# Kernel optimization log

Measured on AMD Instinct MI355X. Metric: run time of the kernel, lower is better.

The kernel has to match this reference:

```python
import jax, jax.numpy as jnp
import numpy as np

N, E = 50000, 800000
IN, EF, D, H = 128, 128, 32, 8
CUTOFF = 5.0
NEG_SLOPE = 0.2


def setup_inputs() -> dict:
    key = jax.random.key(0)
    ks = jax.random.split(key, 14)
    s = 0.1  # param init scale (xavier-ish)
    return {
        "nfeat": jax.random.normal(ks[0], (N, IN), jnp.float32),
        "efeat": jax.random.normal(ks[1], (E, EF), jnp.float32),
        "rij": jax.random.uniform(ks[2], (E,), jnp.float32) * 6.0,
        "src": jax.random.randint(ks[3], (E,), 0, N, jnp.int32),
        "dst": jax.random.randint(ks[4], (E,), 0, N, jnp.int32),
        "W_fc": jax.random.normal(ks[5], (H * D, IN), jnp.float32) * s,
        "W_e1": jax.random.normal(ks[6], (D, EF), jnp.float32) * s,
        "b_e1": jnp.zeros((D,), jnp.float32),
        "W_e2": jax.random.normal(ks[7], (H * D, D), jnp.float32) * s,
        "b_e2": jnp.zeros((H * D,), jnp.float32),
        "attn_l": jax.random.normal(ks[8], (1, H, D), jnp.float32) * s,
        "attn_r": jax.random.normal(ks[9], (1, H, D), jnp.float32) * s,
        "attn_edge": jax.random.normal(ks[10], (1, H, D), jnp.float32) * s,
        "bias": jnp.zeros((H * D,), jnp.float32),
    }


def _ssp(x):
    # ShiftedSoftplus: softplus(x) - log(2)
    return jax.nn.softplus(x) - jnp.log(2.0).astype(x.dtype)


def _cosine_cutoff(r):
    return jnp.where(r < CUTOFF, 0.5 * (jnp.cos(jnp.pi * r / CUTOFF) + 1.0), 0.0)


def reference(nfeat, efeat, rij, src, dst, W_fc, W_e1, b_e1, W_e2, b_e2,
              attn_l, attn_r, attn_edge, bias):
    n = nfeat.shape[0]
    feat = (nfeat @ W_fc.T).reshape(n, H, D)                # [N,H,D]
    ef = _ssp(efeat @ W_e1.T + b_e1)                         # [E,D]
    ef = _ssp(ef @ W_e2.T + b_e2)                            # [E,H*D]
    ef = (_cosine_cutoff(rij)[:, None] * ef).reshape(-1, H, D)  # [E,H,D]

    el = jnp.sum(feat * attn_l, axis=-1)                     # [N,H]
    er = jnp.sum(feat * attn_r, axis=-1)                     # [N,H]
    ee = jnp.sum(ef * attn_edge, axis=-1)                    # [E,H]

    e = jax.nn.leaky_relu(el[src] + er[dst] + ee, NEG_SLOPE)  # [E,H]
    # edge softmax over destination-node neighborhoods
    emax = jax.ops.segment_max(e, dst, num_segments=n)
    ex = jnp.exp(e - emax[dst])
    esum = jax.ops.segment_sum(ex, dst, num_segments=n)
    a = ex / esum[dst]                                       # [E,H]
    a = a * ee                                               # a * dis

    m = feat[src] * a[:, :, None]                            # [E,H,D]
    rst = jax.ops.segment_sum(m, dst, num_segments=n)        # [N,H,D]
    rst = rst + bias.reshape(1, H, D)
    return rst
```

## Files before the change

### kernel.cpp

```cpp
#include <hip/hip_runtime.h>
#include <hip/hip_bf16.h>

#define NN 50000
#define NE 800000
#define HD 256
#define KIN 128
#define SCAN_B 49

#define FB_FEAT 1563
#define FB_FILL 1024
#define FB_EDGE 12500

typedef __attribute__((ext_vector_type(8))) short bf16x8;
typedef __attribute__((ext_vector_type(8))) short short8v;
typedef __attribute__((ext_vector_type(4))) float f32x4;

static __device__ __forceinline__ short f2b(float f){
  union { __hip_bfloat16 h; short s; } u;
  u.h = __float2bfloat16(f);
  return u.s;
}
static __device__ __forceinline__ float b2f(short s){
  union { __hip_bfloat16 h; short s; } u;
  u.s = s;
  return __bfloat162float(u.h);
}
static __device__ __forceinline__ unsigned packbf(float a, float b){
  union { short s[2]; unsigned u; } z;
  z.s[0] = f2b(a); z.s[1] = f2b(b);
  return z.u;
}
static __device__ __forceinline__ float sspf(float x){
#if __has_builtin(__builtin_amdgcn_exp2f) && __has_builtin(__builtin_amdgcn_logf)
  const float t = __builtin_amdgcn_exp2f(fabsf(x) * -1.4426950408889634f);
  return fmaf(__builtin_amdgcn_logf(1.0f + t) - 1.0f, 0.69314718055994531f, fmaxf(x, 0.0f));
#else
  const float t = __expf(-fabsf(x));
  return fmaxf(x, 0.0f) + __logf(1.0f + t) - 0.69314718055994531f;
#endif
}

__global__ void k_cvh(const float* __restrict__ wfc, const float* __restrict__ we1,
                      const float* __restrict__ we2,
                      const float* __restrict__ be2, const float* __restrict__ attn_e,
                      const int* __restrict__ dst,
                      short* __restrict__ wfcb, short* __restrict__ we1b,
                      short* __restrict__ we2b, float* __restrict__ w2pk,
                      int* __restrict__ deg){
  const int i = blockIdx.x*256 + threadIdx.x;
  if (i < HD*KIN) wfcb[i] = f2b(wfc[i]);
  if (i < 32*KIN) we1b[i] = f2b(we1[i]);
  if (i < HD*32)  we2b[i] = f2b(we2[i]);
  if (i < 512){
    const int cht = i >> 5, r = i & 31, lq = r >> 3, j = r & 7;
    const int ch = cht*16 + lq*4 + (j & 3);
    w2pk[i] = (j < 4) ? be2[ch] : attn_e[ch];
  }
  for (int e = i; e < NE; e += gridDim.x*blockDim.x)
    atomicAdd(&deg[dst[e]], 1);
}

__global__ __launch_bounds__(1024) void k_scanA(const int* __restrict__ deg,
                                                int* __restrict__ bsum){
  __shared__ int ws[16];
  const int t = threadIdx.x;
  const int i = blockIdx.x*1024 + t;
  int v = (i < NN) ? deg[i] : 0;
#pragma unroll
  for (int m=1;m<64;m<<=1) v += __shfl_xor(v, m, 64);
  if ((t & 63) == 0) ws[t >> 6] = v;
  __syncthreads();
  if (t == 0){
    int s = 0;
#pragma unroll
    for (int k=0;k<16;++k) s += ws[k];
    bsum[blockIdx.x] = s;
  }
}

__global__ __launch_bounds__(1024) void k_scanC(const int* __restrict__ deg,
                                                const int* __restrict__ bsum,
                                                int* __restrict__ rowptr,
                                                int* __restrict__ fillptr){
  __shared__ int ws[16];
  __shared__ int boff_s, total_s;
  const int t = threadIdx.x, l = t & 63, wid = t >> 6;
  if (t < 64){
    const int v = (t < SCAN_B) ? bsum[t] : 0;
    int x = v;
#pragma unroll
    for (int off=1; off<64; off<<=1){
      const int y = __shfl_up(x, off, 64);
      if (t >= off) x += y;
    }
    if (t == (int)blockIdx.x) boff_s = x - v;
    if (t == SCAN_B-1) total_s = x;
  }
  __syncthreads();
  const int i = blockIdx.x*1024 + t;
  const int v = (i < NN) ? deg[i] : 0;
  int x = v;
#pragma unroll
  for (int off=1; off<64; off<<=1){
    const int y = __shfl_up(x, off, 64);
    if (l >= off) x += y;
  }
  if (l == 63) ws[wid] = x;
  __syncthreads();
  if (t == 0){
    int run = 0;
#pragma unroll
    for (int k=0;k<16;++k){ const int tmp = ws[k]; ws[k] = run; run += tmp; }
  }
  __syncthreads();
  if (i < NN){
    const int excl = boff_s + ws[wid] + (x - v);
    rowptr[i] = excl; fillptr[i] = excl;
  }
  if (blockIdx.x == 0 && t == 0) rowptr[NN] = total_s;
}

static __device__ __forceinline__ void feat_body(
    int bid, int tid,
    const float* __restrict__ nfeat, const short* __restrict__ wfcb,
    const float* __restrict__ attn_l, const float* __restrict__ attn_r,
    short* __restrict__ featb, float* __restrict__ el, float* __restrict__ er)
{
  const int n0 = bid * 32;
  const int w = tid >> 6, l = tid & 63, l15 = l & 15, lq = l >> 4;

  f32x4 acc[2][4];
#pragma unroll
  for (int a=0;a<2;++a)
#pragma unroll
    for (int b=0;b<4;++b) acc[a][b] = (f32x4)0.0f;

#pragma unroll
  for (int ks=0; ks<4; ++ks){
    const int k0 = ks*32 + lq*8;
    bf16x8 af[2];
#pragma unroll
    for (int tr=0; tr<2; ++tr){
      int row = n0 + tr*16 + l15;
      if (row >= NN) row = NN-1;
      const float4 x0 = *reinterpret_cast<const float4*>(nfeat + (size_t)row*KIN + k0);
      const float4 x1 = *reinterpret_cast<const float4*>(nfeat + (size_t)row*KIN + k0 + 4);
      af[tr][0]=f2b(x0.x); af[tr][1]=f2b(x0.y); af[tr][2]=f2b(x0.z); af[tr][3]=f2b(x0.w);
      af[tr][4]=f2b(x1.x); af[tr][5]=f2b(x1.y); af[tr][6]=f2b(x1.z); af[tr][7]=f2b(x1.w);
    }
#pragma unroll
    for (int tc=0; tc<4; ++tc){
      const int c = w*64 + tc*16 + l15;
      const bf16x8 bfrag = *reinterpret_cast<const bf16x8*>(wfcb + c*KIN + k0);
#pragma unroll
      for (int tr=0; tr<2; ++tr)
        acc[tr][tc] = __builtin_amdgcn_mfma_f32_16x16x32_bf16(af[tr], bfrag, acc[tr][tc], 0,0,0);
    }
  }

  float alr[4], arr_[4];
#pragma unroll
  for (int tc=0;tc<4;++tc){
    const int c = w*64 + tc*16 + l15;
    alr[tc] = attn_l[c]; arr_[tc] = attn_r[c];
  }
  float pl[2][4][2], pr[2][4][2];
#pragma unroll
  for (int tr=0;tr<2;++tr)
#pragma unroll
    for (int j=0;j<4;++j){ pl[tr][j][0]=pl[tr][j][1]=0.f; pr[tr][j][0]=pr[tr][j][1]=0.f; }

#pragma unroll
  for (int tr=0;tr<2;++tr){
    const int rowb = tr*16 + lq*4;
#pragma unroll
    for (int tc=0;tc<4;++tc){
      const int c = w*64 + tc*16 + l15;
      const int h2 = tc>>1;
#pragma unroll
      for (int j=0;j<4;++j){
        const float v = acc[tr][tc][j];
        const int node = n0 + rowb + j;
        if (node < NN) featb[node*HD + c] = f2b(v);
        pl[tr][j][h2] += v*alr[tc];
        pr[tr][j][h2] += v*arr_[tc];
      }
    }
  }
#pragma unroll
  for (int m=1;m<16;m<<=1){
#pragma unroll
    for (int tr=0;tr<2;++tr)
#pragma unroll
      for (int j=0;j<4;++j){
        pl[tr][j][0] += __shfl_xor(pl[tr][j][0], m, 64);
        pl[tr][j][1] += __shfl_xor(pl[tr][j][1], m, 64);
        pr[tr][j][0] += __shfl_xor(pr[tr][j][0], m, 64);
        pr[tr][j][1] += __shfl_xor(pr[tr][j][1], m, 64);
      }
  }
#pragma unroll
  for (int tr=0;tr<2;++tr)
#pragma unroll
    for (int j=0;j<4;++j)
      if (l15 == tr*4+j){
        const int node = n0 + tr*16 + lq*4 + j;
        if (node < NN){
          el[node*8 + 2*w + 0] = pl[tr][j][0];
          el[node*8 + 2*w + 1] = pl[tr][j][1];
          er[node*8 + 2*w + 0] = pr[tr][j][0];
          er[node*8 + 2*w + 1] = pr[tr][j][1];
        }
      }
}

static __device__ __forceinline__ void fill_body(
    int bid, int tid,
    const int* __restrict__ dst, const int* __restrict__ src,
    int* __restrict__ fillptr, int2* __restrict__ esrc)
{
  for (int i = bid*256 + tid; i < NE; i += FB_FILL*256){
    const int p = atomicAdd(&fillptr[dst[i]], 1);
    esrc[p] = make_int2(i, src[i]);
  }
}

static __device__ __forceinline__ void edge_body(
    int bid, int tid,
    const float* __restrict__ efeat, const float* __restrict__ rij,
    const short* __restrict__ we1b, const float* __restrict__ be1,
    const short* __restrict__ we2b, const float* __restrict__ w2pk,
    float* __restrict__ ee)
{
  const int w = tid >> 6, l = tid & 63, l15 = l & 15, lq = l >> 4;
  const int e0w = bid * 64 + w * 16;

  const float* erow = efeat + (size_t)(e0w + l15)*KIN + lq*8;
  const float4 r0 = *reinterpret_cast<const float4*>(erow);
  const float4 r1 = *reinterpret_cast<const float4*>(erow + 4);
  const float4 r2 = *reinterpret_cast<const float4*>(erow + 32);
  const float4 r3 = *reinterpret_cast<const float4*>(erow + 36);
  const float4 r4 = *reinterpret_cast<const float4*>(erow + 64);
  const float4 r5 = *reinterpret_cast<const float4*>(erow + 68);
  const float4 r6 = *reinterpret_cast<const float4*>(erow + 96);
  const float4 r7 = *reinterpret_cast<const float4*>(erow + 100);
  const float rv = rij[e0w + l15];

  f32x4 acc_t0 = (f32x4)0.0f, acc_t1 = (f32x4)0.0f;
  float4 raw[8] = {r0,r1,r2,r3,r4,r5,r6,r7};
#pragma unroll
  for (int ks=0; ks<4; ++ks){
    const int k0 = ks*32 + lq*8;
    bf16x8 bfr;
    bfr[0]=f2b(raw[2*ks].x); bfr[1]=f2b(raw[2*ks].y); bfr[2]=f2b(raw[2*ks].z); bfr[3]=f2b(raw[2*ks].w);
    bfr[4]=f2b(raw[2*ks+1].x); bfr[5]=f2b(raw[2*ks+1].y); bfr[6]=f2b(raw[2*ks+1].z); bfr[7]=f2b(raw[2*ks+1].w);
    const bf16x8 a0 = *reinterpret_cast<const bf16x8*>(we1b + (l15     )*KIN + k0);
    const bf16x8 a1 = *reinterpret_cast<const bf16x8*>(we1b + (16 + l15)*KIN + k0);
    acc_t0 = __builtin_amdgcn_mfma_f32_16x16x32_bf16(a0, bfr, acc_t0, 0,0,0);
    acc_t1 = __builtin_amdgcn_mfma_f32_16x16x32_bf16(a1, bfr, acc_t1, 0,0,0);
  }

  const f32x4 b1a = *reinterpret_cast<const f32x4*>(be1 + lq*4);
  const f32x4 b1b = *reinterpret_cast<const f32x4*>(be1 + 16 + lq*4);
  const unsigned t0lo = packbf(sspf(acc_t0[0]+b1a[0]), sspf(acc_t0[1]+b1a[1]));
  const unsigned t0hi = packbf(sspf(acc_t0[2]+b1a[2]), sspf(acc_t0[3]+b1a[3]));
  const unsigned t1lo = packbf(sspf(acc_t1[0]+b1b[0]), sspf(acc_t1[1]+b1b[1]));
  const unsigned t1hi = packbf(sspf(acc_t1[2]+b1b[2]), sspf(acc_t1[3]+b1b[3]));

  const int srcA = ((lq & 1) << 5) + l15;
  const int srcB = srcA + 16;
  const int a_lo0 = __shfl((int)t0lo, srcA, 64), a_hi0 = __shfl((int)t0hi, srcA, 64);
  const int b_lo0 = __shfl((int)t0lo, srcB, 64), b_hi0 = __shfl((int)t0hi, srcB, 64);
  const int a_lo1 = __shfl((int)t1lo, srcA, 64), a_hi1 = __shfl((int)t1hi, srcA, 64);
  const int b_lo1 = __shfl((int)t1lo, srcB, 64), b_hi1 = __shfl((int)t1hi, srcB, 64);
  const bool th1sel = (lq & 2);
  union { int u[4]; bf16x8 v; } bx;
  bx.u[0] = th1sel ? a_lo1 : a_lo0;
  bx.u[1] = th1sel ? a_hi1 : a_hi0;
  bx.u[2] = th1sel ? b_lo1 : b_lo0;
  bx.u[3] = th1sel ? b_hi1 : b_hi0;

  const float* pkb = w2pk + lq*8;
  float pe[8];
#pragma unroll
  for (int h=0;h<8;++h) pe[h] = 0.f;
#pragma unroll
  for (int cht=0; cht<16; ++cht){
    const bf16x8 a2 = *reinterpret_cast<const bf16x8*>(we2b + (cht*16 + l15)*32 + lq*8);
    const f32x4 d = __builtin_amdgcn_mfma_f32_16x16x32_bf16(a2, bx.v, (f32x4)0.0f, 0,0,0);
    const f32x4 b2v = *reinterpret_cast<const f32x4*>(pkb + cht*32);
    const f32x4 aev = *reinterpret_cast<const f32x4*>(pkb + cht*32 + 4);
    float s = 0.f;
#pragma unroll
    for (int j=0;j<4;++j) s = fmaf(sspf(d[j] + b2v[j]), aev[j], s);
    pe[cht>>1] += s;
  }
#pragma unroll
  for (int h=0;h<8;++h){
    pe[h] += __shfl_xor(pe[h], 16, 64);
    pe[h] += __shfl_xor(pe[h], 32, 64);
  }
  const float fcv = (rv < 5.0f) ? 0.5f*(__cosf(0.62831853071795864f*rv) + 1.0f) : 0.0f;
  const float o0 = (lq==0) ? pe[0] : (lq==1) ? pe[2] : (lq==2) ? pe[4] : pe[6];
  const float o1 = (lq==0) ? pe[1] : (lq==1) ? pe[3] : (lq==2) ? pe[5] : pe[7];
  float2 outv; outv.x = o0*fcv; outv.y = o1*fcv;
  *reinterpret_cast<float2*>(ee + (size_t)(e0w + l15)*8 + lq*2) = outv;
}

__global__ __launch_bounds__(256, 4) void k_big(
    const float* __restrict__ nfeat, const short* __restrict__ wfcb,
    const float* __restrict__ attn_l, const float* __restrict__ attn_r,
    short* __restrict__ featb, float* __restrict__ el, float* __restrict__ er,
    const int* __restrict__ dst, const int* __restrict__ src,
    int* __restrict__ fillptr, int2* __restrict__ esrc,
    const float* __restrict__ efeat, const float* __restrict__ rij,
    const short* __restrict__ we1b, const float* __restrict__ be1,
    const short* __restrict__ we2b, const float* __restrict__ w2pk,
    float* __restrict__ ee)
{
  const int bid = blockIdx.x, tid = threadIdx.x;
  if (bid < FB_FEAT){
    feat_body(bid, tid, nfeat, wfcb, attn_l, attn_r, featb, el, er);
  } else if (bid < FB_FEAT + FB_FILL){
    fill_body(bid - FB_FEAT, tid, dst, src, fillptr, esrc);
  } else {
    edge_body(bid - FB_FEAT - FB_FILL, tid, efeat, rij, we1b, be1, we2b, w2pk, ee);
  }
}

__global__ __launch_bounds__(256) void k_sa(
    const int* __restrict__ rowptr, const int2* __restrict__ esrc,
    const float* __restrict__ el, const float* __restrict__ er,
    const float* __restrict__ ee, const short* __restrict__ featb,
    const float* __restrict__ bias, float* __restrict__ out)
{
  const int t = threadIdx.x, l = t & 63, w = t >> 6;
  const int n = blockIdx.x*4 + w;
  const int beg = rowptr[n], end = rowptr[n+1];
  const int stream = l >> 5, cl = l & 31, hh = cl >> 2;
  const float er_hh = er[(size_t)n*8 + hh];

  float acc[8];
#pragma unroll
  for (int k=0;k<8;++k) acc[k] = 0.f;
  float s = 0.f;
  for (int p = beg + stream; p < end; p += 2){
    const int2 es = esrc[p];
    const float x = ee[(size_t)es.x*8 + hh];
    float e = x + el[(size_t)es.y*8 + hh] + er_hh;
    e = e > 0.f ? e : 0.2f*e;
    const float pex = __expf(e);
    const float c = pex * x;
    s += pex;
    const short8v fv = *reinterpret_cast<const short8v*>(featb + (size_t)es.y*HD + cl*8);
#pragma unroll
    for (int k=0;k<8;++k) acc[k] = fmaf(c, b2f(fv[k]), acc[k]);
  }
  s += __shfl_xor(s, 32, 64);
#pragma unroll
  for (int k=0;k<8;++k) acc[k] += __shfl_xor(acc[k], 32, 64);
  if (l < 32){
    const float inv = (s > 0.f) ? 1.0f / s : 0.0f;
    const float4 b0 = *reinterpret_cast<const float4*>(bias + cl*8);
    const float4 b1 = *reinterpret_cast<const float4*>(bias + cl*8 + 4);
    float4 o0, o1;
    o0.x=fmaf(acc[0],inv,b0.x); o0.y=fmaf(acc[1],inv,b0.y);
    o0.z=fmaf(acc[2],inv,b0.z); o0.w=fmaf(acc[3],inv,b0.w);
    o1.x=fmaf(acc[4],inv,b1.x); o1.y=fmaf(acc[5],inv,b1.y);
    o1.z=fmaf(acc[6],inv,b1.z); o1.w=fmaf(acc[7],inv,b1.w);
    *reinterpret_cast<float4*>(out + (size_t)n*HD + cl*8) = o0;
    *reinterpret_cast<float4*>(out + (size_t)n*HD + cl*8 + 4) = o1;
  }
}

extern "C" void kernel_launch(void* const* d_in, const int* in_sizes, int n_in,
                              void* d_out, int out_size, void* d_ws, size_t ws_size,
                              hipStream_t stream) {
  const float* nfeat  = (const float*)d_in[0];
  const float* efeat  = (const float*)d_in[1];
  const float* rij    = (const float*)d_in[2];
  const int*   src    = (const int*)d_in[3];
  const int*   dst    = (const int*)d_in[4];
  const float* W_fc   = (const float*)d_in[5];
  const float* W_e1   = (const float*)d_in[6];
  const float* b_e1   = (const float*)d_in[7];
  const float* W_e2   = (const float*)d_in[8];
  const float* b_e2   = (const float*)d_in[9];
  const float* attn_l = (const float*)d_in[10];
  const float* attn_r = (const float*)d_in[11];
  const float* attn_e = (const float*)d_in[12];
  const float* bias   = (const float*)d_in[13];
  float* out = (float*)d_out;

  size_t off = 0;
  auto carve = [&](size_t nbytes) -> void* {
    void* p = (char*)d_ws + off;
    off += (nbytes + 255) & ~(size_t)255;
    return p;
  };
  short* featb = (short*)carve((size_t)NN*HD*2);
  float* el    = (float*)carve((size_t)NN*8*4);
  float* er    = (float*)carve((size_t)NN*8*4);
  float* ee    = (float*)carve((size_t)NE*8*4);
  int* deg     = (int*)carve((size_t)NN*4);
  int* rowptr  = (int*)carve((size_t)(NN+1)*4);
  int* fillptr = (int*)carve((size_t)(NN+1)*4);
  int2* esrc   = (int2*)carve((size_t)NE*8);
  int* bsum    = (int*)carve((size_t)SCAN_B*4);
  short* wfcb  = (short*)carve((size_t)HD*KIN*2);
  short* we1b  = (short*)carve((size_t)32*KIN*2);
  short* we2b  = (short*)carve((size_t)HD*32*2);
  float* w2pk  = (float*)carve((size_t)512*4);

  hipMemsetAsync(deg, 0, (size_t)NN*4, stream);
  k_cvh<<<1024, 256, 0, stream>>>(W_fc, W_e1, W_e2, b_e2, attn_e, dst,
                                  wfcb, we1b, we2b, w2pk, deg);
  k_scanA<<<SCAN_B, 1024, 0, stream>>>(deg, bsum);
  k_scanC<<<SCAN_B, 1024, 0, stream>>>(deg, bsum, rowptr, fillptr);
  k_big<<<FB_FEAT + FB_FILL + FB_EDGE, 256, 0, stream>>>(
      nfeat, wfcb, attn_l, attn_r, featb, el, er,
      dst, src, fillptr, esrc,
      efeat, rij, we1b, b_e1, we2b, w2pk, ee);
  k_sa<<<(NN+3)/4, 256, 0, stream>>>(rowptr, esrc, el, er, ee, featb, bias, out);
}
```

Measured before the change: 376.4 us.

## Process two edge tiles per wave and schedule edge blocks first

Each wave in the edge MLP path now handles 32 edges instead of 16, so every weight fragment load from we1b and we2b feeds two MFMAs, and the edge block count is halved. All 16 efeat float4 loads are issued up front for more memory-level parallelism. The fused kernel now dispatches edge blocks first, then feature, then fill. The occupancy hint in launch_bounds is dropped. Register pressure roughly doubles in the edge path, which may cut occupancy.

```diff
diff --git a/kernel.cpp b/kernel.cpp
--- a/kernel.cpp
+++ b/kernel.cpp
@@ -7,9 +7,9 @@
 #define KIN 128
 #define SCAN_B 49
 
+#define FB_EDGE 6250
 #define FB_FEAT 1563
 #define FB_FILL 1024
-#define FB_EDGE 12500
 
 typedef __attribute__((ext_vector_type(8))) short bf16x8;
 typedef __attribute__((ext_vector_type(8))) short short8v;
@@ -29,6 +29,12 @@
   union { short s[2]; unsigned u; } z;
   z.s[0] = f2b(a); z.s[1] = f2b(b);
   return z.u;
+}
+static __device__ __forceinline__ bf16x8 cvt8(float4 x0, float4 x1){
+  bf16x8 t;
+  t[0]=f2b(x0.x); t[1]=f2b(x0.y); t[2]=f2b(x0.z); t[3]=f2b(x0.w);
+  t[4]=f2b(x1.x); t[5]=f2b(x1.y); t[6]=f2b(x1.z); t[7]=f2b(x1.w);
+  return t;
 }
 static __device__ __forceinline__ float sspf(float x){
 #if __has_builtin(__builtin_amdgcn_exp2f) && __has_builtin(__builtin_amdgcn_logf)
@@ -145,8 +151,7 @@
       if (row >= NN) row = NN-1;
       const float4 x0 = *reinterpret_cast<const float4*>(nfeat + (size_t)row*KIN + k0);
       const float4 x1 = *reinterpret_cast<const float4*>(nfeat + (size_t)row*KIN + k0 + 4);
-      af[tr][0]=f2b(x0.x); af[tr][1]=f2b(x0.y); af[tr][2]=f2b(x0.z); af[tr][3]=f2b(x0.w);
-      af[tr][4]=f2b(x1.x); af[tr][5]=f2b(x1.y); af[tr][6]=f2b(x1.z); af[tr][7]=f2b(x1.w);
+      af[tr] = cvt8(x0, x1);
     }
 #pragma unroll
     for (int tc=0; tc<4; ++tc){
@@ -233,81 +238,121 @@
     float* __restrict__ ee)
 {
   const int w = tid >> 6, l = tid & 63, l15 = l & 15, lq = l >> 4;
-  const int e0w = bid * 64 + w * 16;
-
-  const float* erow = efeat + (size_t)(e0w + l15)*KIN + lq*8;
-  const float4 r0 = *reinterpret_cast<const float4*>(erow);
-  const float4 r1 = *reinterpret_cast<const float4*>(erow + 4);
-  const float4 r2 = *reinterpret_cast<const float4*>(erow + 32);
-  const float4 r3 = *reinterpret_cast<const float4*>(erow + 36);
-  const float4 r4 = *reinterpret_cast<const float4*>(erow + 64);
-  const float4 r5 = *reinterpret_cast<const float4*>(erow + 68);
-  const float4 r6 = *reinterpret_cast<const float4*>(erow + 96);
-  const float4 r7 = *reinterpret_cast<const float4*>(erow + 100);
-  const float rv = rij[e0w + l15];
-
-  f32x4 acc_t0 = (f32x4)0.0f, acc_t1 = (f32x4)0.0f;
-  float4 raw[8] = {r0,r1,r2,r3,r4,r5,r6,r7};
+  const int e0w = bid * 128 + w * 32;
+
+  const float* erowA = efeat + (size_t)(e0w + l15)*KIN + lq*8;
+  const float* erowB = erowA + (size_t)16*KIN;
+  const float4 a0_ = *reinterpret_cast<const float4*>(erowA);
+  const float4 a1_ = *reinterpret_cast<const float4*>(erowA + 4);
+  const float4 a2_ = *reinterpret_cast<const float4*>(erowA + 32);
+  const float4 a3_ = *reinterpret_cast<const float4*>(erowA + 36);
+  const float4 a4_ = *reinterpret_cast<const float4*>(erowA + 64);
+  const float4 a5_ = *reinterpret_cast<const float4*>(erowA + 68);
+  const float4 a6_ = *reinterpret_cast<const float4*>(erowA + 96);
+  const float4 a7_ = *reinterpret_cast<const float4*>(erowA + 100);
+  const float4 b0_ = *reinterpret_cast<const float4*>(erowB);
+  const float4 b1_ = *reinterpret_cast<const float4*>(erowB + 4);
+  const float4 b2_ = *reinterpret_cast<const float4*>(erowB + 32);
+  const float4 b3_ = *reinterpret_cast<const float4*>(erowB + 36);
+  const float4 b4_ = *reinterpret_cast<const float4*>(erowB + 64);
+  const float4 b5_ = *reinterpret_cast<const float4*>(erowB + 68);
+  const float4 b6_ = *reinterpret_cast<const float4*>(erowB + 96);
+  const float4 b7_ = *reinterpret_cast<const float4*>(erowB + 100);
+  const float rvA = rij[e0w + l15];
+  const float rvB = rij[e0w + 16 + l15];
+
+  bf16x8 bfA[4], bfB[4];
+  bfA[0]=cvt8(a0_,a1_); bfA[1]=cvt8(a2_,a3_); bfA[2]=cvt8(a4_,a5_); bfA[3]=cvt8(a6_,a7_);
+  bfB[0]=cvt8(b0_,b1_); bfB[1]=cvt8(b2_,b3_); bfB[2]=cvt8(b4_,b5_); bfB[3]=cvt8(b6_,b7_);
+
+  f32x4 aA0=(f32x4)0.f, aA1=(f32x4)0.f, aB0=(f32x4)0.f, aB1=(f32x4)0.f;
 #pragma unroll
   for (int ks=0; ks<4; ++ks){
     const int k0 = ks*32 + lq*8;
-    bf16x8 bfr;
-    bfr[0]=f2b(raw[2*ks].x); bfr[1]=f2b(raw[2*ks].y); bfr[2]=f2b(raw[2*ks].z); bfr[3]=f2b(raw[2*ks].w);
-    bfr[4]=f2b(raw[2*ks+1].x); bfr[5]=f2b(raw[2*ks+1].y); bfr[6]=f2b(raw[2*ks+1].z); bfr[7]=f2b(raw[2*ks+1].w);
-    const bf16x8 a0 = *reinterpret_cast<const bf16x8*>(we1b + (l15     )*KIN + k0);
-    const bf16x8 a1 = *reinterpret_cast<const bf16x8*>(we1b + (16 + l15)*KIN + k0);
-    acc_t0 = __builtin_amdgcn_mfma_f32_16x16x32_bf16(a0, bfr, acc_t0, 0,0,0);
-    acc_t1 = __builtin_amdgcn_mfma_f32_16x16x32_bf16(a1, bfr, acc_t1, 0,0,0);
+    const bf16x8 w0 = *reinterpret_cast<const bf16x8*>(we1b + (l15     )*KIN + k0);
+    const bf16x8 w1 = *reinterpret_cast<const bf16x8*>(we1b + (16 + l15)*KIN + k0);
+    aA0 = __builtin_amdgcn_mfma_f32_16x16x32_bf16(w0, bfA[ks], aA0, 0,0,0);
+    aA1 = __builtin_amdgcn_mfma_f32_16x16x32_bf16(w1, bfA[ks], aA1, 0,0,0);
+    aB0 = __builtin_amdgcn_mfma_f32_16x16x32_bf16(w0, bfB[ks], aB0, 0,0,0);
+    aB1 = __builtin_amdgcn_mfma_f32_16x16x32_bf16(w1, bfB[ks], aB1, 0,0,0);
   }
 
   const f32x4 b1a = *reinterpret_cast<const f32x4*>(be1 + lq*4);
   const f32x4 b1b = *reinterpret_cast<const f32x4*>(be1 + 16 + lq*4);
-  const unsigned t0lo = packbf(sspf(acc_t0[0]+b1a[0]), sspf(acc_t0[1]+b1a[1]));
-  const unsigned t0hi = packbf(sspf(acc_t0[2]+b1a[2]), sspf(acc_t0[3]+b1a[3]));
-  const unsigned t1lo = packbf(sspf(acc_t1[0]+b1b[0]), sspf(acc_t1[1]+b1b[1]));
-  const unsigned t1hi = packbf(sspf(acc_t1[2]+b1b[2]), sspf(acc_t1[3]+b1b[3]));
+  const unsigned At0lo = packbf(sspf(aA0[0]+b1a[0]), sspf(aA0[1]+b1a[1]));
+  const unsigned At0hi = packbf(sspf(aA0[2]+b1a[2]), sspf(aA0[3]+b1a[3]));
+  const unsigned At1lo = packbf(sspf(aA1[0]+b1b[0]), sspf(aA1[1]+b1b[1]));
+  const unsigned At1hi = packbf(sspf(aA1[2]+b1b[2]), sspf(aA1[3]+b1b[3]));
+  const unsigned Bt0lo = packbf(sspf(aB0[0]+b1a[0]), sspf(aB0[1]+b1a[1]));
+  const unsigned Bt0hi = packbf(sspf(aB0[2]+b1a[2]), sspf(aB0[3]+b1a[3]));
+  const unsigned Bt1lo = packbf(sspf(aB1[0]+b1b[0]), sspf(aB1[1]+b1b[1]));
+  const unsigned Bt1hi = packbf(sspf(aB1[2]+b1b[2]), sspf(aB1[3]+b1b[3]));
 
   const int srcA = ((lq & 1) << 5) + l15;
   const int srcB = srcA + 16;
-  const int a_lo0 = __shfl((int)t0lo, srcA, 64), a_hi0 = __shfl((int)t0hi, srcA, 64);
-  const int b_lo0 = __shfl((int)t0lo, srcB, 64), b_hi0 = __shfl((int)t0hi, srcB, 64);
-  const int a_lo1 = __shfl((int)t1lo, srcA, 64), a_hi1 = __shfl((int)t1hi, srcA, 64);
-  const int b_lo1 = __shfl((int)t1lo, srcB, 64), b_hi1 = __shfl((int)t1hi, srcB, 64);
   const bool th1sel = (lq & 2);
-  union { int u[4]; bf16x8 v; } bx;
-  bx.u[0] = th1sel ? a_lo1 : a_lo0;
-  bx.u[1] = th1sel ? a_hi1 : a_hi0;
-  bx.u[2] = th1sel ? b_lo1 : b_lo0;
-  bx.u[3] = th1sel ? b_hi1 : b_hi0;
+  union { int u[4]; bf16x8 v; } bxA, bxB;
+  {
+    const int x0 = __shfl((int)At0lo, srcA, 64), x1 = __shfl((int)At0hi, srcA, 64);
+    const int x2 = __shfl((int)At0lo, srcB, 64), x3 = __shfl((int)At0hi, srcB, 64);
+    const int y0 = __shfl((int)At1lo, srcA, 64), y1 = __shfl((int)At1hi, srcA, 64);
+    const int y2 = __shfl((int)At1lo, srcB, 64), y3 = __shfl((int)At1hi, srcB, 64);
+    bxA.u[0] = th1sel ? y0 : x0;
+    bxA.u[1] = th1sel ? y1 : x1;
+    bxA.u[2] = th1sel ? y2 : x2;
+    bxA.u[3] = th1sel ? y3 : x3;
+  }
+  {
+    const int x0 = __shfl((int)Bt0lo, srcA, 64), x1 = __shfl((int)Bt0hi, srcA, 64);
+    const int x2 = __shfl((int)Bt0lo, srcB, 64), x3 = __shfl((int)Bt0hi, srcB, 64);
+    const int y0 = __shfl((int)Bt1lo, srcA, 64), y1 = __shfl((int)Bt1hi, srcA, 64);
+    const int y2 = __shfl((int)Bt1lo, srcB, 64), y3 = __shfl((int)Bt1hi, srcB, 64);
+    bxB.u[0] = th1sel ? y0 : x0;
+    bxB.u[1] = th1sel ? y1 : x1;
+    bxB.u[2] = th1sel ? y2 : x2;
+    bxB.u[3] = th1sel ? y3 : x3;
+  }
 
   const float* pkb = w2pk + lq*8;
-  float pe[8];
-#pragma unroll
-  for (int h=0;h<8;++h) pe[h] = 0.f;
+  float peA[8], peB[8];
+#pragma unroll
+  for (int h=0;h<8;++h){ peA[h]=0.f; peB[h]=0.f; }
 #pragma unroll
   for (int cht=0; cht<16; ++cht){
     const bf16x8 a2 = *reinterpret_cast<const bf16x8*>(we2b + (cht*16 + l15)*32 + lq*8);
-    const f32x4 d = __builtin_amdgcn_mfma_f32_16x16x32_bf16(a2, bx.v, (f32x4)0.0f, 0,0,0);
+    const f32x4 dA = __builtin_amdgcn_mfma_f32_16x16x32_bf16(a2, bxA.v, (f32x4)0.0f, 0,0,0);
+    const f32x4 dB = __builtin_amdgcn_mfma_f32_16x16x32_bf16(a2, bxB.v, (f32x4)0.0f, 0,0,0);
     const f32x4 b2v = *reinterpret_cast<const f32x4*>(pkb + cht*32);
     const f32x4 aev = *reinterpret_cast<const f32x4*>(pkb + cht*32 + 4);
-    float s = 0.f;
-#pragma unroll
-    for (int j=0;j<4;++j) s = fmaf(sspf(d[j] + b2v[j]), aev[j], s);
-    pe[cht>>1] += s;
+    float sA = 0.f, sB = 0.f;
+#pragma unroll
+    for (int j=0;j<4;++j){
+      sA = fmaf(sspf(dA[j] + b2v[j]), aev[j], sA);
+      sB = fmaf(sspf(dB[j] + b2v[j]), aev[j], sB);
+    }
+    peA[cht>>1] += sA;
+    peB[cht>>1] += sB;
   }
 #pragma unroll
   for (int h=0;h<8;++h){
-    pe[h] += __shfl_xor(pe[h], 16, 64);
-    pe[h] += __shfl_xor(pe[h], 32, 64);
-  }
-  const float fcv = (rv < 5.0f) ? 0.5f*(__cosf(0.62831853071795864f*rv) + 1.0f) : 0.0f;
-  const float o0 = (lq==0) ? pe[0] : (lq==1) ? pe[2] : (lq==2) ? pe[4] : pe[6];
-  const float o1 = (lq==0) ? pe[1] : (lq==1) ? pe[3] : (lq==2) ? pe[5] : pe[7];
-  float2 outv; outv.x = o0*fcv; outv.y = o1*fcv;
-  *reinterpret_cast<float2*>(ee + (size_t)(e0w + l15)*8 + lq*2) = outv;
-}
-
-__global__ __launch_bounds__(256, 4) void k_big(
+    peA[h] += __shfl_xor(peA[h], 16, 64);
+    peA[h] += __shfl_xor(peA[h], 32, 64);
+    peB[h] += __shfl_xor(peB[h], 16, 64);
+    peB[h] += __shfl_xor(peB[h], 32, 64);
+  }
+  const float fcA = (rvA < 5.0f) ? 0.5f*(__cosf(0.62831853071795864f*rvA) + 1.0f) : 0.0f;
+  const float fcB = (rvB < 5.0f) ? 0.5f*(__cosf(0.62831853071795864f*rvB) + 1.0f) : 0.0f;
+  const float oA0 = (lq==0) ? peA[0] : (lq==1) ? peA[2] : (lq==2) ? peA[4] : peA[6];
+  const float oA1 = (lq==0) ? peA[1] : (lq==1) ? peA[3] : (lq==2) ? peA[5] : peA[7];
+  const float oB0 = (lq==0) ? peB[0] : (lq==1) ? peB[2] : (lq==2) ? peB[4] : peB[6];
+  const float oB1 = (lq==0) ? peB[1] : (lq==1) ? peB[3] : (lq==2) ? peB[5] : peB[7];
+  float2 ovA; ovA.x = oA0*fcA; ovA.y = oA1*fcA;
+  float2 ovB; ovB.x = oB0*fcB; ovB.y = oB1*fcB;
+  *reinterpret_cast<float2*>(ee + (size_t)(e0w + l15)*8 + lq*2) = ovA;
+  *reinterpret_cast<float2*>(ee + (size_t)(e0w + 16 + l15)*8 + lq*2) = ovB;
+}
+
+__global__ __launch_bounds__(256) void k_big(
     const float* __restrict__ nfeat, const short* __restrict__ wfcb,
     const float* __restrict__ attn_l, const float* __restrict__ attn_r,
     short* __restrict__ featb, float* __restrict__ el, float* __restrict__ er,
@@ -319,12 +364,12 @@
     float* __restrict__ ee)
 {
   const int bid = blockIdx.x, tid = threadIdx.x;
-  if (bid < FB_FEAT){
-    feat_body(bid, tid, nfeat, wfcb, attn_l, attn_r, featb, el, er);
-  } else if (bid < FB_FEAT + FB_FILL){
-    fill_body(bid - FB_FEAT, tid, dst, src, fillptr, esrc);
+  if (bid < FB_EDGE){
+    edge_body(bid, tid, efeat, rij, we1b, be1, we2b, w2pk, ee);
+  } else if (bid < FB_EDGE + FB_FEAT){
+    feat_body(bid - FB_EDGE, tid, nfeat, wfcb, attn_l, attn_r, featb, el, er);
   } else {
-    edge_body(bid - FB_FEAT - FB_FILL, tid, efeat, rij, we1b, be1, we2b, w2pk, ee);
+    fill_body(bid - FB_EDGE - FB_FEAT, tid, dst, src, fillptr, esrc);
   }
 }
 
@@ -417,7 +462,7 @@
                                   wfcb, we1b, we2b, w2pk, deg);
   k_scanA<<<SCAN_B, 1024, 0, stream>>>(deg, bsum);
   k_scanC<<<SCAN_B, 1024, 0, stream>>>(deg, bsum, rowptr, fillptr);
-  k_big<<<FB_FEAT + FB_FILL + FB_EDGE, 256, 0, stream>>>(
+  k_big<<<FB_EDGE + FB_FEAT + FB_FILL, 256, 0, stream>>>(
       nfeat, wfcb, attn_l, attn_r, featb, el, er,
       dst, src, fillptr, esrc,
       efeat, rij, we1b, b_e1, we2b, w2pk, ee);
```

Measured after the change: 401.3 us. 1.07x slower.
